# Optimization experiments

Measured on AMD Instinct MI355X. Metric: run time of the kernel, lower is better.

The kernel has to match this reference:

```python
import math
import jax, jax.numpy as jnp
import numpy as np

B, T = 2, 2048
D_MODEL, D_HEAD = 2048, 128
N_Q, N_KV = 16, 4
QPG = N_Q // N_KV  # queries per kv group
ROPE_BASE = 10000.0
YARN_SCALE = 4.0
ORIG_MAX_LEN = 4096
BETA_FAST, BETA_SLOW = 32.0, 1.0
RMS_EPS = 1.1920929e-07  # torch.finfo(float32).eps (nn.RMSNorm default)


def _yarn_inv_freq():
    inv = 1.0 / ROPE_BASE ** (np.arange(0, D_HEAD, 2, dtype=np.float32) / D_HEAD)
    wavelengths = 2.0 * math.pi / inv
    low_wavelen = ORIG_MAX_LEN / BETA_SLOW
    high_wavelen = ORIG_MAX_LEN / BETA_FAST
    gamma = np.clip((low_wavelen - wavelengths) / (low_wavelen - high_wavelen), 0.0, 1.0)
    return (gamma * inv + (1.0 - gamma) * inv / YARN_SCALE).astype(np.float32)

INV_FREQ = jnp.asarray(_yarn_inv_freq())  # (D_HEAD//2,) constant buffer
MSCALE = 0.1 * math.log(YARN_SCALE) + 1.0
ATTN_SCALE = 1.0 / (MSCALE * math.sqrt(D_HEAD))


def _rms_norm(x, w):
    # normalize over last dim (d_head), learnable per-dim weight
    return x * jax.lax.rsqrt(jnp.mean(x * x, axis=-1, keepdims=True) + RMS_EPS) * w


def _apply_rope(x):
    # x: (..., T, d_head)
    t = jnp.arange(x.shape[-2], dtype=jnp.float32)
    freqs = jnp.outer(t, INV_FREQ)                 # (T, d/2)
    emb = jnp.concatenate([freqs, freqs], axis=-1)  # (T, d)
    cos, sin = jnp.cos(emb), jnp.sin(emb)
    half = x.shape[-1] // 2
    x_rot = jnp.concatenate([-x[..., half:], x[..., :half]], axis=-1)
    return x * cos + x_rot * sin


def setup_inputs() -> dict:
    key = jax.random.key(0)
    ks = jax.random.split(key, 5)
    x = jax.random.normal(ks[0], (B, T, D_MODEL), dtype=jnp.float32)
    w_scale = 0.02
    Wq = jax.random.normal(ks[1], (D_MODEL, N_Q * D_HEAD), dtype=jnp.float32) * w_scale
    Wkv = jax.random.normal(ks[2], (D_MODEL, 2 * N_KV * D_HEAD), dtype=jnp.float32) * w_scale
    Wo = jax.random.normal(ks[3], (N_Q * D_HEAD, D_MODEL), dtype=jnp.float32) * w_scale
    q_norm_w = jnp.ones((D_HEAD,), dtype=jnp.float32)
    k_norm_w = jnp.ones((D_HEAD,), dtype=jnp.float32)
    return {"x": x, "Wq": Wq, "Wkv": Wkv, "Wo": Wo,
            "q_norm_w": q_norm_w, "k_norm_w": k_norm_w}


def reference(x, Wq, Wkv, Wo, q_norm_w, k_norm_w):
    b, t, _ = x.shape
    # projections
    q = (x @ Wq).reshape(b, t, QPG, N_KV, D_HEAD).transpose(0, 2, 3, 1, 4)  # (b,qpg,g,t,d)
    kv = x @ Wkv
    k, v = jnp.split(kv, 2, axis=-1)
    k = k.reshape(b, t, N_KV, D_HEAD).transpose(0, 2, 1, 3)  # (b,g,t,d)
    v = v.reshape(b, t, N_KV, D_HEAD).transpose(0, 2, 1, 3)  # (b,g,t,d)
    # RMSNorm + YaRN RoPE on q,k (math done in float32 as in source)
    q = _apply_rope(_rms_norm(q, q_norm_w))
    k = _apply_rope(_rms_norm(k, k_norm_w))
    # GQA replication: head index h = qpg*N_KV + g (matches source rearrange/reshape)
    q = q.reshape(b, N_Q, t, D_HEAD)
    k = jnp.broadcast_to(k[:, None], (b, QPG, N_KV, t, D_HEAD)).reshape(b, N_Q, t, D_HEAD)
    v = jnp.broadcast_to(v[:, None], (b, QPG, N_KV, t, D_HEAD)).reshape(b, N_Q, t, D_HEAD)
    # causal SDPA with custom scale
    scores = jnp.einsum('bhtd,bhsd->bhts', q, k) * ATTN_SCALE
    causal = jnp.tril(jnp.ones((t, t), dtype=bool))
    scores = jnp.where(causal, scores, jnp.finfo(scores.dtype).min)
    probs = jax.nn.softmax(scores, axis=-1)
    attn = jnp.einsum('bhts,bhsd->bhtd', probs, v)
    out = attn.transpose(0, 2, 1, 3).reshape(b, t, N_Q * D_HEAD)
    return out @ Wo
```

## Files before the change

kernel.cpp:

```cpp
#include <hip/hip_runtime.h>
#include <cmath>

typedef float f32x4 __attribute__((ext_vector_type(4)));
typedef __bf16 bf16x8 __attribute__((ext_vector_type(8)));

#define DEV static __device__ __forceinline__

DEV unsigned short f2bf(float f) {
  unsigned int u = __builtin_bit_cast(unsigned int, f);
  u += 0x7FFFu + ((u >> 16) & 1u);
  return (unsigned short)(u >> 16);
}
DEV float bf2f(unsigned short h) {
  unsigned int u = ((unsigned int)h) << 16;
  return __builtin_bit_cast(float, u);
}
DEV unsigned int cvtpk(float lo, float hi) {
  unsigned int r;
  asm("v_cvt_pk_bf16_f32 %0, %1, %2" : "=v"(r) : "v"(lo), "v"(hi));
  return r;
}
DEV f32x4 mfma16(bf16x8 a, bf16x8 b, f32x4 c) {
  return __builtin_amdgcn_mfma_f32_16x16x32_bf16(a, b, c, 0, 0, 0);
}
DEV void dma16(const void* g, void* l) {
  __builtin_amdgcn_global_load_lds(
      (const __attribute__((address_space(1))) void*)(uintptr_t)g,
      (__attribute__((address_space(3))) void*)(unsigned int)(uintptr_t)l,
      16, 0, 0);
}

constexpr int T_SEQ = 2048;

__global__ __launch_bounds__(256) void prep_all(const float4* __restrict__ in,
                                                ushort* __restrict__ out,
                                                float2* __restrict__ rope,
                                                const float* __restrict__ Wq,
                                                const float* __restrict__ Wkv,
                                                const float* __restrict__ Wo,
                                                ushort* __restrict__ wqkv,
                                                ushort* __restrict__ wot) {
  __shared__ ushort tile[64][65];
  const int bx = blockIdx.x;
  if (bx < 8192) {
    int i = bx * 256 + threadIdx.x;
    float4 v = in[i];
    unsigned int lo = (unsigned int)f2bf(v.x) | ((unsigned int)f2bf(v.y) << 16);
    unsigned int hi = (unsigned int)f2bf(v.z) | ((unsigned int)f2bf(v.w) << 16);
    int row = i >> 9;
    int e = (i * 4) & 2047;
    size_t o = ((size_t)row << 11) + (size_t)(e ^ ((row & 7) << 3));
    *(uint2*)(out + o) = make_uint2(lo, hi);
  } else if (bx < 8704) {
    int gid = (bx - 8192) * 256 + threadIdx.x;
    int t = gid >> 6, i = gid & 63;
    double inv = pow(10000.0, -((double)(2 * i)) / 128.0);
    double wl = 6.283185307179586 / inv;
    double gm = (4096.0 - wl) / (4096.0 - 128.0);
    gm = gm < 0.0 ? 0.0 : (gm > 1.0 ? 1.0 : gm);
    float f = (float)(gm * inv + (1.0 - gm) * inv * 0.25);
    float th = (float)t * f;
    float s, c;
    sincosf(th, &s, &c);
    rope[gid] = make_float2(c, s);
  } else {
    const int l = bx - 8704;
    const int bxl0 = l % 80, by = l / 80;
    const float* src;
    ushort* dst;
    int C, bxl;
    if (bxl0 < 32) {
      src = Wq; dst = wqkv; C = 2048; bxl = bxl0;
    } else if (bxl0 < 48) {
      src = Wkv; dst = wqkv + (size_t)2048 * 2048; C = 1024; bxl = bxl0 - 32;
    } else {
      src = Wo; dst = wot; C = 2048; bxl = bxl0 - 48;
    }
    const int R = 2048;
    int c0 = bxl * 64, r0 = by * 64;
    int j = threadIdx.x & 63, i0 = threadIdx.x >> 6;
#pragma unroll
    for (int ii = 0; ii < 16; ++ii) {
      int i = i0 + ii * 4;
      tile[i][j] = f2bf(src[(size_t)(r0 + i) * C + c0 + j]);
    }
    __syncthreads();
#pragma unroll
    for (int ii = 0; ii < 16; ++ii) {
      int jr = i0 + ii * 4;
      dst[(size_t)(c0 + jr) * R + ((r0 + j) ^ ((jr & 7) << 3))] = tile[j][jr];
    }
  }
}

template <int BM, int BN, int OUT_BF16>
__global__ __launch_bounds__(512) void gemm256(const ushort* __restrict__ A,
                                               const ushort* __restrict__ Bt,
                                               void* __restrict__ Cv,
                                               int M, int N, int K) {
  constexpr int MT = BM / 32;
  constexpr int NT = BN / 64;
  constexpr int ADMA = BM / 64;
  constexpr int BDMA = BN / 64;
  constexpr int BC0 = (BDMA + 1) / 2;
  __shared__ ushort lA[2][BM * 64];
  __shared__ ushort lB[2][BN * 64];
  const int tid = threadIdx.x, lane = tid & 63, w = tid >> 6;
  const int wm = (w >> 2) * (BM / 2);
  const int wn = (w & 3) * (BN / 4);
  const int bid = blockIdx.x;
  const int f = ((bid & 7) << 6) + (bid >> 3);
  const int pm = f >> 4, pn = f & 15;
  const int m0 = pm * BM, n0 = pn * BN;

  f32x4 acc[MT][NT] = {};

  const size_t K2 = (size_t)K * 2;
  const char* Ab = (const char*)A + (size_t)m0 * K2;
  const char* Bb = (const char*)Bt + (size_t)n0 * K2;
  const int srb = lane >> 3;
  const int scb = (lane & 7) * 16;

  auto stageA = [&](int t, int bi) {
#pragma unroll
    for (int ii = 0; ii < ADMA; ++ii) {
      const int ar = w * (BM / 8) + ii * 8;
      dma16(Ab + (size_t)(ar + srb) * K2 + (size_t)t * 128 + scb,
            (char*)lA[bi] + ar * 128);
    }
  };
  auto stageB = [&](int t, int bi, int l0, int cnt) {
    for (int ii = l0; ii < l0 + cnt; ++ii) {
      const int br = w * (BN / 8) + ii * 8;
      dma16(Bb + (size_t)(br + srb) * K2 + (size_t)t * 128 + scb,
            (char*)lB[bi] + br * 128);
    }
  };

  stageA(0, 0);
  stageB(0, 0, 0, BDMA);
  const int nkt = K >> 6;

  asm volatile("s_waitcnt vmcnt(0)" ::: "memory");
  __builtin_amdgcn_s_barrier();

  for (int t = 0; t < nkt; ++t) {
    const int cur = t & 1;
    const char* lAc = (const char*)lA[cur];
    const char* lBc = (const char*)lB[cur];
    const bool pre = (t + 1 < nkt);

    bf16x8 af[2][MT];
#pragma unroll
    for (int ph = 0; ph < NT; ++ph) {
      if (ph == 0) {
#pragma unroll
        for (int kk = 0; kk < 2; ++kk) {
          const int byo = kk * 64 + ((lane >> 4) << 4);
#pragma unroll
          for (int i = 0; i < MT; ++i) {
            int row = wm + i * 16 + (lane & 15);
            af[kk][i] = *(const bf16x8*)(lAc + row * 128 + (byo ^ ((row & 7) << 4)));
          }
        }
      }
      bf16x8 bfr[2];
#pragma unroll
      for (int kk = 0; kk < 2; ++kk) {
        const int byo = kk * 64 + ((lane >> 4) << 4);
        int row = wn + ph * 16 + (lane & 15);
        bfr[kk] = *(const bf16x8*)(lBc + row * 128 + (byo ^ ((row & 7) << 4)));
      }
      if (pre) {
        if (ph == 0) {
          stageA(t + 1, cur ^ 1);
          stageB(t + 1, cur ^ 1, 0, BC0);
        } else if (ph == 1) {
          stageB(t + 1, cur ^ 1, BC0, BDMA - BC0);
        }
      }
      __builtin_amdgcn_s_barrier();
      __builtin_amdgcn_sched_barrier(0);
      __builtin_amdgcn_s_setprio(1);
#pragma unroll
      for (int kk = 0; kk < 2; ++kk)
#pragma unroll
        for (int i = 0; i < MT; ++i)
          acc[i][ph] = mfma16(af[kk][i], bfr[kk], acc[i][ph]);
      __builtin_amdgcn_s_setprio(0);
    }
    __builtin_amdgcn_sched_barrier(0);
    asm volatile("s_waitcnt vmcnt(0)" ::: "memory");
    __builtin_amdgcn_s_barrier();
  }

  const int rr = (lane >> 4) << 2;
  const int cc = lane & 15;
  if (OUT_BF16) {
    ushort* C = (ushort*)Cv;
#pragma unroll
    for (int mt = 0; mt < MT; ++mt)
#pragma unroll
      for (int nt = 0; nt < NT; ++nt)
#pragma unroll
        for (int j = 0; j < 4; ++j) {
          int r = m0 + wm + mt * 16 + rr + j;
          int c = n0 + wn + nt * 16 + cc;
          C[(size_t)r * N + c] = f2bf(acc[mt][nt][j]);
        }
  } else {
    float* C = (float*)Cv;
#pragma unroll
    for (int mt = 0; mt < MT; ++mt)
#pragma unroll
      for (int nt = 0; nt < NT; ++nt)
#pragma unroll
        for (int j = 0; j < 4; ++j) {
          int r = m0 + wm + mt * 16 + rr + j;
          int c = n0 + wn + nt * 16 + cc;
          C[(size_t)r * N + c] = acc[mt][nt][j];
        }
  }
}

__global__ __launch_bounds__(256) void normrope_tv(const ushort* __restrict__ qkv,
                                                   const float* __restrict__ qw,
                                                   const float* __restrict__ kw,
                                                   const float2* __restrict__ rope,
                                                   ushort* __restrict__ qout,
                                                   ushort* __restrict__ kout,
                                                   ushort* __restrict__ vt,
                                                   float q_scale) {
  __shared__ ushort tile[64][65];
  const int bx = blockIdx.x;
  if (bx < 20480) {
    const int w = threadIdx.x >> 6, lane = threadIdx.x & 63;
    const int vi = bx * 4 + w;
    const ushort* src;
    const float* wt;
    ushort* dst;
    float extra;
    int t, bb;
    if (vi < 65536) {
      int row = vi >> 4, H = vi & 15;
      bb = row >> 11;
      t = row & 2047;
      src = qkv + (size_t)row * 3072 + H * 128 + lane * 2;
      wt = qw;
      extra = q_scale;
      dst = qout + ((size_t)(bb * 16 + H) * T_SEQ + t) * 128 + lane * 2;
    } else {
      int vi2 = vi - 65536;
      int row = vi2 >> 2, gg = vi2 & 3;
      bb = row >> 11;
      t = row & 2047;
      src = qkv + (size_t)row * 3072 + 2048 + gg * 128 + lane * 2;
      wt = kw;
      extra = 1.f;
      dst = kout + ((size_t)(bb * 4 + gg) * T_SEQ + t) * 128 +
            ((lane * 2) ^ ((t & 7) << 3));
    }
    float x0 = bf2f(src[0]), x1 = bf2f(src[1]);
    float ss = x0 * x0 + x1 * x1;
#pragma unroll
    for (int d = 1; d < 64; d <<= 1) ss += __shfl_xor(ss, d, 64);
    float sc = rsqrtf(ss * (1.f / 128.f) + 1.1920929e-7f);
    float w0 = wt[lane * 2], w1 = wt[lane * 2 + 1];
    float xn0 = x0 * sc * w0, xn1 = x1 * sc * w1;
    float p0 = __shfl_xor(xn0, 32, 64), p1 = __shfl_xor(xn1, 32, 64);
    float r0 = lane < 32 ? -p0 : p0;
    float r1 = lane < 32 ? -p1 : p1;
    int i0 = (lane * 2) & 63;
    float2 cs0 = rope[t * 64 + i0];
    float2 cs1 = rope[t * 64 + i0 + 1];
    float o0 = (xn0 * cs0.x + r0 * cs0.y) * extra;
    float o1 = (xn1 * cs1.x + r1 * cs1.y) * extra;
    unsigned int pkv = (unsigned int)f2bf(o0) | ((unsigned int)f2bf(o1) << 16);
    *(unsigned int*)dst = pkv;
  } else {
    const int l = bx - 20480;
    int t0 = (l & 31) * 64;
    int y = l >> 5;
    int dh = y & 1, bg = y >> 1;
    int bb = bg >> 2, g = bg & 3;
    int j = threadIdx.x & 63, i0 = threadIdx.x >> 6;
#pragma unroll
    for (int ii = 0; ii < 16; ++ii) {
      int i = i0 + ii * 4;
      tile[i][j] = qkv[(size_t)(bb * T_SEQ + t0 + i) * 3072 + 2560 + g * 128 + dh * 64 + j];
    }
    __syncthreads();
#pragma unroll
    for (int ii = 0; ii < 16; ++ii) {
      int jr = i0 + ii * 4;
      vt[((size_t)bg * 128 + dh * 64 + jr) * T_SEQ + ((t0 + j) ^ ((jr & 7) << 3))] = tile[j][jr];
    }
  }
}

__global__ __launch_bounds__(256, 2) void attn_fwd(const ushort* __restrict__ qh,
                                                   const ushort* __restrict__ kh,
                                                   const ushort* __restrict__ vt,
                                                   ushort* __restrict__ o) {
  const int f = blockIdx.x;
  const int half = f >> 8, c = f & 255;
  const int kk = c >> 5, bh = c & 31;
  const int qt = half ? kk : (15 - kk);
  const int b = bh >> 4, H = bh & 15;
  const int g = H & 3;
  const int tid = threadIdx.x, lane = tid & 63, w = tid >> 6;
  const int wrow0 = qt * 128 + w * 32;

  __shared__ ushort lK[2][64 * 128];
  __shared__ ushort lV[2][128 * 64];
  __shared__ ushort lP[4 * 32 * 64];

  bf16x8 qf[2][4];
#pragma unroll
  for (int mt = 0; mt < 2; ++mt) {
    const ushort* qb = qh + ((size_t)(b * 16 + H) * T_SEQ + wrow0 + mt * 16 + (lane & 15)) * 128 +
                       ((lane >> 4) << 3);
#pragma unroll
    for (int kc = 0; kc < 4; ++kc) qf[mt][kc] = *(const bf16x8*)(qb + kc * 32);
  }

  f32x4 oacc[2][8] = {};
  float mrow[2] = {-INFINITY, -INFINITY};
  float lrow[2] = {0.f, 0.f};

  const char* kpl = (const char*)(kh + (size_t)(b * 4 + g) * T_SEQ * 128);
  const char* vpl = (const char*)(vt + (size_t)(b * 4 + g) * 128 * T_SEQ);

  auto stage = [&](int j, int bi) {
#pragma unroll
    for (int ii = 0; ii < 4; ++ii) {
      const int off = w * 4096 + ii * 1024;
      dma16(kpl + (size_t)j * 16384 + off + lane * 16, (char*)lK[bi] + off);
      const int vrow = w * 32 + ii * 8 + (lane >> 3);
      dma16(vpl + (size_t)vrow * (T_SEQ * 2) + j * 128 + (lane & 7) * 16,
            (char*)lV[bi] + off);
    }
  };

  stage(0, 0);

  const int rsel = ((lane >> 4) << 2);

  const int jmax = 2 * qt + 1;
  for (int j = 0; j <= jmax; ++j) {
    const int cur = j & 1;
    if (j < jmax) {
      stage(j + 1, cur ^ 1);
      asm volatile("s_waitcnt vmcnt(8)" ::: "memory");
    } else {
      asm volatile("s_waitcnt vmcnt(0)" ::: "memory");
    }
    __builtin_amdgcn_s_barrier();
    __builtin_amdgcn_sched_barrier(0);

    f32x4 s[2][4];
#pragma unroll
    for (int nt = 0; nt < 4; ++nt) {
      bf16x8 kf[4];
      int krow = nt * 16 + (lane & 15);
#pragma unroll
      for (int kc = 0; kc < 4; ++kc) {
        int byo = kc * 64 + ((lane >> 4) << 4);
        kf[kc] = *(const bf16x8*)((const char*)lK[cur] + krow * 256 + (byo ^ ((krow & 7) << 4)));
      }
#pragma unroll
      for (int mt = 0; mt < 2; ++mt) {
        f32x4 a = {0.f, 0.f, 0.f, 0.f};
#pragma unroll
        for (int kc = 0; kc < 4; ++kc) a = mfma16(kf[kc], qf[mt][kc], a);
        s[mt][nt] = a;
      }
    }

    if (j * 64 + 63 > wrow0) {
#pragma unroll
      for (int mt = 0; mt < 2; ++mt) {
        int qrow = wrow0 + mt * 16 + (lane & 15);
#pragma unroll
        for (int nt = 0; nt < 4; ++nt)
#pragma unroll
          for (int jj = 0; jj < 4; ++jj) {
            int col = j * 64 + nt * 16 + rsel + jj;
            if (col > qrow) s[mt][nt][jj] = -3.0e38f;
          }
      }
    }

    float pmx[2], mn[2];
#pragma unroll
    for (int mt = 0; mt < 2; ++mt) {
      float a0 = fmaxf(fmaxf(s[mt][0][0], s[mt][0][1]), fmaxf(s[mt][0][2], s[mt][0][3]));
      float a1 = fmaxf(fmaxf(s[mt][1][0], s[mt][1][1]), fmaxf(s[mt][1][2], s[mt][1][3]));
      float a2 = fmaxf(fmaxf(s[mt][2][0], s[mt][2][1]), fmaxf(s[mt][2][2], s[mt][2][3]));
      float a3 = fmaxf(fmaxf(s[mt][3][0], s[mt][3][1]), fmaxf(s[mt][3][2], s[mt][3][3]));
      float p = fmaxf(fmaxf(a0, a1), fmaxf(a2, a3));
      p = fmaxf(p, __shfl_xor(p, 16, 64));
      p = fmaxf(p, __shfl_xor(p, 32, 64));
      pmx[mt] = p;
      mn[mt] = mrow[mt];
    }

    bool ok = (pmx[0] <= mrow[0] + 11.5417f) && (pmx[1] <= mrow[1] + 11.5417f);
    if (!__all(ok)) {
#pragma unroll
      for (int mt = 0; mt < 2; ++mt) {
        mn[mt] = fmaxf(mrow[mt], pmx[mt]);
        float rsc = exp2f(mrow[mt] - mn[mt]);
        mrow[mt] = mn[mt];
        lrow[mt] *= rsc;
        float rr0 = __shfl(rsc, rsel + 0, 64);
        float rr1 = __shfl(rsc, rsel + 1, 64);
        float rr2 = __shfl(rsc, rsel + 2, 64);
        float rr3 = __shfl(rsc, rsel + 3, 64);
#pragma unroll
        for (int dt = 0; dt < 8; ++dt) {
          oacc[mt][dt][0] *= rr0; oacc[mt][dt][1] *= rr1;
          oacc[mt][dt][2] *= rr2; oacc[mt][dt][3] *= rr3;
        }
      }
    }

#pragma unroll
    for (int mt = 0; mt < 2; ++mt) {
      float ps = 0.f;
      int prow = mt * 16 + (lane & 15);
      char* pbase = (char*)lP + w * 4096 + prow * 128;
      int swz = (prow & 7) << 4;
#pragma unroll
      for (int nt = 0; nt < 4; ++nt) {
        float p0 = exp2f(s[mt][nt][0] - mn[mt]);
        float p1 = exp2f(s[mt][nt][1] - mn[mt]);
        float p2 = exp2f(s[mt][nt][2] - mn[mt]);
        float p3 = exp2f(s[mt][nt][3] - mn[mt]);
        ps += (p0 + p1) + (p2 + p3);
        int pcb = (nt * 32 + ((lane >> 4) << 3)) ^ swz;
        *(uint2*)(pbase + pcb) = make_uint2(cvtpk(p0, p1), cvtpk(p2, p3));
      }
      ps += __shfl_xor(ps, 16, 64);
      ps += __shfl_xor(ps, 32, 64);
      lrow[mt] += ps;
    }

#pragma unroll
    for (int kc2 = 0; kc2 < 2; ++kc2) {
      bf16x8 pa[2];
#pragma unroll
      for (int mt = 0; mt < 2; ++mt) {
        int prow = mt * 16 + (lane & 15);
        int pbo = kc2 * 64 + ((lane >> 4) << 4);
        pa[mt] = *(const bf16x8*)((char*)lP + w * 4096 + prow * 128 + (pbo ^ ((prow & 7) << 4)));
      }
#pragma unroll
      for (int dt = 0; dt < 8; ++dt) {
        int vrow = dt * 16 + (lane & 15);
        int vbo = kc2 * 64 + ((lane >> 4) << 4);
        bf16x8 vf = *(const bf16x8*)((const char*)lV[cur] + vrow * 128 + (vbo ^ ((vrow & 7) << 4)));
#pragma unroll
        for (int mt = 0; mt < 2; ++mt) oacc[mt][dt] = mfma16(pa[mt], vf, oacc[mt][dt]);
      }
    }

    __builtin_amdgcn_sched_barrier(0);
    __builtin_amdgcn_s_barrier();
  }

#pragma unroll
  for (int mt = 0; mt < 2; ++mt) {
    float linv = 1.f / lrow[mt];
    float iv0 = __shfl(linv, rsel + 0, 64);
    float iv1 = __shfl(linv, rsel + 1, 64);
    float iv2 = __shfl(linv, rsel + 2, 64);
    float iv3 = __shfl(linv, rsel + 3, 64);
    int row = wrow0 + mt * 16 + rsel;
#pragma unroll
    for (int dt = 0; dt < 8; ++dt) {
      int col = H * 128 + dt * 16 + (lane & 15);
      o[(size_t)(b * T_SEQ + row + 0) * 2048 + (col ^ (((row + 0) & 7) << 3))] =
          f2bf(oacc[mt][dt][0] * iv0);
      o[(size_t)(b * T_SEQ + row + 1) * 2048 + (col ^ (((row + 1) & 7) << 3))] =
          f2bf(oacc[mt][dt][1] * iv1);
      o[(size_t)(b * T_SEQ + row + 2) * 2048 + (col ^ (((row + 2) & 7) << 3))] =
          f2bf(oacc[mt][dt][2] * iv2);
      o[(size_t)(b * T_SEQ + row + 3) * 2048 + (col ^ (((row + 3) & 7) << 3))] =
          f2bf(oacc[mt][dt][3] * iv3);
    }
  }
}

extern "C" void kernel_launch(void* const* d_in, const int* in_sizes, int n_in,
                              void* d_out, int out_size, void* d_ws, size_t ws_size,
                              hipStream_t stream) {
  (void)in_sizes; (void)n_in; (void)out_size; (void)ws_size;
  const float* x = (const float*)d_in[0];
  const float* Wq = (const float*)d_in[1];
  const float* Wkv = (const float*)d_in[2];
  const float* Wo = (const float*)d_in[3];
  const float* qnw = (const float*)d_in[4];
  const float* knw = (const float*)d_in[5];
  float* out = (float*)d_out;
  char* ws = (char*)d_ws;

  ushort* xb = (ushort*)(ws);
  ushort* wqkv = (ushort*)(ws + 16777216);
  ushort* wot = (ushort*)(ws + 29360128);
  ushort* qkvraw = (ushort*)(ws + 37748736);
  ushort* kh = (ushort*)(ws + 62914560);
  ushort* vtp = (ushort*)(ws + 67108864);
  float2* rope = (float2*)(ws + 71303168);
  ushort* qh = xb;
  ushort* attnb = qkvraw;

  float attn_scale = 1.0f / ((0.1f * logf(4.0f) + 1.0f) * sqrtf(128.0f));
  float q_scale = attn_scale * 1.44269504f;

  prep_all<<<11264, 256, 0, stream>>>((const float4*)x, xb, rope, Wq, Wkv, Wo, wqkv, wot);
  gemm256<128, 192, 1><<<512, 512, 0, stream>>>(xb, wqkv, qkvraw, 4096, 3072, 2048);
  normrope_tv<<<20992, 256, 0, stream>>>(qkvraw, qnw, knw, rope, qh, kh, vtp, q_scale);
  attn_fwd<<<512, 256, 0, stream>>>(qh, kh, vtp, attnb);
  gemm256<128, 128, 0><<<512, 512, 0, stream>>>(attnb, wot, out, 4096, 2048, 2048);
}
```

Before: 195.5 us.

## Switch projection GEMM to 32x32x16 MFMA with new wave tiling

Replaces the 16x16x32 bf16 MFMA in the projection GEMM with the 32x32x16 variant and re-partitions the 8 waves. Each wave now owns 32 rows and BN/2 columns instead of BM/2 by BN/4. The LDS fragment loads and the output store index mapping are rewritten to match the 32x32 accumulator layout. The aim is fewer MFMA issues and fewer LDS reads per FLOP. In exchange it adds accumulator register pressure and needs BM to be exactly 128 for the 4x32 row split, otherwise rows are left uncovered.

```diff
diff --git a/kernel.cpp b/kernel.cpp
--- a/kernel.cpp
+++ b/kernel.cpp
@@ -2,6 +2,7 @@
 #include <cmath>
 
 typedef float f32x4 __attribute__((ext_vector_type(4)));
+typedef float f32x16 __attribute__((ext_vector_type(16)));
 typedef __bf16 bf16x8 __attribute__((ext_vector_type(8)));
 
 #define DEV static __device__ __forceinline__
@@ -22,6 +23,9 @@
 }
 DEV f32x4 mfma16(bf16x8 a, bf16x8 b, f32x4 c) {
   return __builtin_amdgcn_mfma_f32_16x16x32_bf16(a, b, c, 0, 0, 0);
+}
+DEV f32x16 mfma32(bf16x8 a, bf16x8 b, f32x16 c) {
+  return __builtin_amdgcn_mfma_f32_32x32x16_bf16(a, b, c, 0, 0, 0);
 }
 DEV void dma16(const void* g, void* l) {
   __builtin_amdgcn_global_load_lds(
@@ -98,22 +102,22 @@
                                                const ushort* __restrict__ Bt,
                                                void* __restrict__ Cv,
                                                int M, int N, int K) {
-  constexpr int MT = BM / 32;
-  constexpr int NT = BN / 64;
+  constexpr int NF = BN / 64;
   constexpr int ADMA = BM / 64;
   constexpr int BDMA = BN / 64;
   constexpr int BC0 = (BDMA + 1) / 2;
   __shared__ ushort lA[2][BM * 64];
   __shared__ ushort lB[2][BN * 64];
   const int tid = threadIdx.x, lane = tid & 63, w = tid >> 6;
-  const int wm = (w >> 2) * (BM / 2);
-  const int wn = (w & 3) * (BN / 4);
+  const int hi = lane >> 5, l31 = lane & 31;
+  const int wm = (w >> 1) * 32;
+  const int wn = (w & 1) * (BN / 2);
   const int bid = blockIdx.x;
   const int f = ((bid & 7) << 6) + (bid >> 3);
   const int pm = f >> 4, pn = f & 15;
   const int m0 = pm * BM, n0 = pn * BN;
 
-  f32x4 acc[MT][NT] = {};
+  f32x16 acc[NF] = {};
 
   const size_t K2 = (size_t)K * 2;
   const char* Ab = (const char*)A + (size_t)m0 * K2;
@@ -144,33 +148,29 @@
   asm volatile("s_waitcnt vmcnt(0)" ::: "memory");
   __builtin_amdgcn_s_barrier();
 
+  const int arow = wm + l31;
+  const int aswz = (arow & 7) << 4;
+
   for (int t = 0; t < nkt; ++t) {
     const int cur = t & 1;
     const char* lAc = (const char*)lA[cur];
     const char* lBc = (const char*)lB[cur];
     const bool pre = (t + 1 < nkt);
 
-    bf16x8 af[2][MT];
-#pragma unroll
-    for (int ph = 0; ph < NT; ++ph) {
+    bf16x8 af[4];
+#pragma unroll
+    for (int ph = 0; ph < NF; ++ph) {
       if (ph == 0) {
 #pragma unroll
-        for (int kk = 0; kk < 2; ++kk) {
-          const int byo = kk * 64 + ((lane >> 4) << 4);
-#pragma unroll
-          for (int i = 0; i < MT; ++i) {
-            int row = wm + i * 16 + (lane & 15);
-            af[kk][i] = *(const bf16x8*)(lAc + row * 128 + (byo ^ ((row & 7) << 4)));
-          }
-        }
-      }
-      bf16x8 bfr[2];
-#pragma unroll
-      for (int kk = 0; kk < 2; ++kk) {
-        const int byo = kk * 64 + ((lane >> 4) << 4);
-        int row = wn + ph * 16 + (lane & 15);
-        bfr[kk] = *(const bf16x8*)(lBc + row * 128 + (byo ^ ((row & 7) << 4)));
-      }
+        for (int c = 0; c < 4; ++c)
+          af[c] = *(const bf16x8*)(lAc + arow * 128 + ((c * 32 + 16 * hi) ^ aswz));
+      }
+      bf16x8 bfr[4];
+      const int brow = wn + ph * 32 + l31;
+      const int bswz = (brow & 7) << 4;
+#pragma unroll
+      for (int c = 0; c < 4; ++c)
+        bfr[c] = *(const bf16x8*)(lBc + brow * 128 + ((c * 32 + 16 * hi) ^ bswz));
       if (pre) {
         if (ph == 0) {
           stageA(t + 1, cur ^ 1);
@@ -183,10 +183,7 @@
       __builtin_amdgcn_sched_barrier(0);
       __builtin_amdgcn_s_setprio(1);
 #pragma unroll
-      for (int kk = 0; kk < 2; ++kk)
-#pragma unroll
-        for (int i = 0; i < MT; ++i)
-          acc[i][ph] = mfma16(af[kk][i], bfr[kk], acc[i][ph]);
+      for (int c = 0; c < 4; ++c) acc[ph] = mfma32(af[c], bfr[c], acc[ph]);
       __builtin_amdgcn_s_setprio(0);
     }
     __builtin_amdgcn_sched_barrier(0);
@@ -194,32 +191,28 @@
     __builtin_amdgcn_s_barrier();
   }
 
-  const int rr = (lane >> 4) << 2;
-  const int cc = lane & 15;
   if (OUT_BF16) {
     ushort* C = (ushort*)Cv;
 #pragma unroll
-    for (int mt = 0; mt < MT; ++mt)
-#pragma unroll
-      for (int nt = 0; nt < NT; ++nt)
-#pragma unroll
-        for (int j = 0; j < 4; ++j) {
-          int r = m0 + wm + mt * 16 + rr + j;
-          int c = n0 + wn + nt * 16 + cc;
-          C[(size_t)r * N + c] = f2bf(acc[mt][nt][j]);
-        }
+    for (int nf = 0; nf < NF; ++nf) {
+      const int n = n0 + wn + nf * 32 + l31;
+#pragma unroll
+      for (int r = 0; r < 16; ++r) {
+        const int m = m0 + wm + (r & 3) + 8 * (r >> 2) + 4 * hi;
+        C[(size_t)m * N + n] = f2bf(acc[nf][r]);
+      }
+    }
   } else {
     float* C = (float*)Cv;
 #pragma unroll
-    for (int mt = 0; mt < MT; ++mt)
-#pragma unroll
-      for (int nt = 0; nt < NT; ++nt)
-#pragma unroll
-        for (int j = 0; j < 4; ++j) {
-          int r = m0 + wm + mt * 16 + rr + j;
-          int c = n0 + wn + nt * 16 + cc;
-          C[(size_t)r * N + c] = acc[mt][nt][j];
-        }
+    for (int nf = 0; nf < NF; ++nf) {
+      const int n = n0 + wn + nf * 32 + l31;
+#pragma unroll
+      for (int r = 0; r < 16; ++r) {
+        const int m = m0 + wm + (r & 3) + 8 * (r >> 2) + 4 * hi;
+        C[(size_t)m * N + n] = acc[nf][r];
+      }
+    }
   }
 }
 
```

After: 210.6 us. 1.08x slower.
